# Kernel tuning notes

Hardware: AMD Instinct MI355X
Metric: run time of the kernel (lower is better)

The kernel has to match this reference:

```python
import jax, jax.numpy as jnp
import numpy as np

C_PER_GROUP = 16
T_ITERS = 5
EPS = 1e-5


def setup_inputs() -> dict:
    key = jax.random.key(0)
    k1, = jax.random.split(key, 1)
    N, C, H, W = 32, 256, 64, 64
    x = jax.random.normal(k1, (N, C, H, W), dtype=jnp.float32)
    return {
        "x": x,
        "sw_mean_weight": jnp.ones((2,), jnp.float32),
        "sw_var_weight": jnp.ones((2,), jnp.float32),
        "weight": jnp.ones((C,), jnp.float32),
        "bias": jnp.zeros((C,), jnp.float32),
    }


def reference(x, sw_mean_weight, sw_var_weight, weight, bias):
    N, C, H, W = x.shape
    c = C_PER_GROUP
    g = C // c
    HW = H * W
    NHW = N * HW

    # --- BW (batch whitening) stats over all N,H,W per group (world_size=1) ---
    # torch: x.transpose(0,1).view(g, c, N*H*W)
    xt = jnp.transpose(x, (1, 0, 2, 3)).reshape(g, c, NHW)
    mean_bn = jnp.mean(xt, axis=-1, keepdims=True)              # (g, c, 1)
    xc = xt - mean_bn
    cov_bn = jnp.einsum('gci,gdi->gcd', xc, xc) / NHW           # (g, c, c)

    # broadcast BN stats to (N*g, ...)
    mean_bn_b = jnp.broadcast_to(mean_bn[None], (N, g, c, 1)).reshape(N * g, c, 1)
    cov_bn_b = jnp.broadcast_to(cov_bn[None], (N, g, c, c)).reshape(N * g, c, c)

    # --- IW (instance whitening) stats per (sample, group) ---
    in_data = x.reshape(N * g, c, HW)
    mean_in = jnp.mean(in_data, axis=-1, keepdims=True)         # (N*g, c, 1)
    x_in = in_data - mean_in
    cov_in = jnp.einsum('bci,bdi->bcd', x_in, x_in) / HW        # (N*g, c, c)

    eye = jnp.eye(c, dtype=x.dtype)

    # --- switchable mixing (sw_type = 2: BW + IW) ---
    mw = jax.nn.softmax(sw_mean_weight)
    vw = jax.nn.softmax(sw_var_weight)
    mean = mw[0] * mean_bn_b + mw[1] * mean_in                  # (N*g, c, 1)
    cov = vw[0] * cov_bn_b + vw[1] * cov_in + EPS * eye         # (N*g, c, c)

    # --- Newton-Schulz iterative whitening ---
    trace = jnp.trace(cov, axis1=-2, axis2=-1)[:, None, None]   # (N*g, 1, 1)
    rTr = 1.0 / trace
    cov_N = cov * rTr
    P = jnp.broadcast_to(eye, cov.shape)
    for _ in range(T_ITERS):
        P3 = jnp.matmul(jnp.matmul(P, P), P)
        P = 1.5 * P - 0.5 * jnp.matmul(P3, cov_N)
    wm = P * jnp.sqrt(rTr)                                      # (N*g, c, c)

    x_hat = jnp.matmul(wm, in_data - mean).reshape(N, C, H, W)
    x_hat = x_hat * weight[None, :, None, None] + bias[None, :, None, None]
    return x_hat
```

## Files before the change

kernel.cpp:

```cpp
#include <hip/hip_runtime.h>
#include <stdint.h>

#define HWSZ 4096
#define NTRI 136
#define NSTAT 152
#define NINST 512
#define GCNT 16
#define EPSW 1e-5f
#define CHUNK 512
#define NCHUNK 8

typedef float v2f __attribute__((ext_vector_type(2)));
typedef float v4f __attribute__((ext_vector_type(4)));

typedef __attribute__((address_space(3))) float lds_f;
typedef const __attribute__((address_space(1))) float glb_f;

__device__ __forceinline__ void stage_chunk(const float* __restrict__ xb,
                                            float* bufp, int wv, int lane, int ck) {
#pragma unroll
  for (int ii = 0; ii < 8; ++ii) {
    const int d = wv * 4 + (ii >> 1);
    const int q = ii & 1;
    __builtin_amdgcn_global_load_lds(
        (glb_f*)(xb + (size_t)d * HWSZ + (size_t)ck * CHUNK + q * 256 + lane * 4),
        (lds_f*)(bufp + d * CHUNK + q * 256), 16, 0, 0);
  }
}

__global__ __launch_bounds__(256, 2) void k_inst_stats(const float* __restrict__ x,
                                                       float* __restrict__ inst_stats) {
  const int b = blockIdx.x;
  const int t = threadIdx.x;
  const int lane = t & 63;
  const int wv = t >> 6;

  __shared__ float buf[2][16 * CHUNK];
  __shared__ float red[4 * NSTAT];

  const float* xb = x + (size_t)b * 16 * HWSZ;

  float s1[16];
  float s2[NTRI];
#pragma unroll
  for (int i = 0; i < 16; ++i) s1[i] = 0.f;
#pragma unroll
  for (int i = 0; i < NTRI; ++i) s2[i] = 0.f;

  stage_chunk(xb, &buf[0][0], wv, lane, 0);
  __syncthreads();

#pragma unroll 1
  for (int ck = 0; ck < NCHUNK; ++ck) {
    if (ck + 1 < NCHUNK) stage_chunk(xb, &buf[(ck + 1) & 1][0], wv, lane, ck + 1);
    const float* bc = &buf[ck & 1][0];
    v2f v[16];
#pragma unroll
    for (int d = 0; d < 16; ++d) v[d] = *(const v2f*)&bc[d * CHUNK + 2 * t];
#pragma unroll
    for (int c = 0; c < 16; ++c) s1[c] += v[c].x + v[c].y;
    int tri = 0;
#pragma unroll
    for (int c = 0; c < 16; ++c) {
#pragma unroll
      for (int d = c; d < 16; ++d) {
        s2[tri] += v[c].x * v[d].x + v[c].y * v[d].y;
        ++tri;
      }
    }
    __syncthreads();
  }

#pragma unroll
  for (int q = 0; q < 16; ++q) {
    float v = s1[q];
#pragma unroll
    for (int off = 32; off > 0; off >>= 1) v += __shfl_down(v, off);
    if (lane == 0) red[wv * NSTAT + q] = v;
  }
#pragma unroll
  for (int q = 0; q < NTRI; ++q) {
    float v = s2[q];
#pragma unroll
    for (int off = 32; off > 0; off >>= 1) v += __shfl_down(v, off);
    if (lane == 0) red[wv * NSTAT + 16 + q] = v;
  }
  __syncthreads();
  if (t < NSTAT) {
    inst_stats[(size_t)b * NSTAT + t] =
        red[t] + red[NSTAT + t] + red[2 * NSTAT + t] + red[3 * NSTAT + t];
  }
}

__global__ __launch_bounds__(256) void k_newton(const float* __restrict__ inst_stats,
                                                const float* __restrict__ swm,
                                                const float* __restrict__ swv,
                                                const float* __restrict__ weight,
                                                const float* __restrict__ bias,
                                                float* __restrict__ apply_wm,
                                                float* __restrict__ apply_ofs) {
  const int b = blockIdx.x;
  const int g = b & 15;
  const int t = threadIdx.x;
  const int r = t >> 4;
  const int c = t & 15;

  __shared__ float P[256], Qm[256], Rm[256], CN[256], Wl[256];
  __shared__ float Mm[16], Mi[16], Mb[16];
  __shared__ float Gs[NSTAT];

  if (t < NSTAT) {
    float s = 0.f;
#pragma unroll 8
    for (int n = 0; n < 32; ++n) s += inst_stats[(size_t)(n * GCNT + g) * NSTAT + t];
    Gs[t] = s;
  }

  float a0 = swm[0], a1 = swm[1];
  float mx = fmaxf(a0, a1);
  float e0 = expf(a0 - mx), e1 = expf(a1 - mx);
  const float mw0 = e0 / (e0 + e1), mw1 = e1 / (e0 + e1);
  a0 = swv[0]; a1 = swv[1];
  mx = fmaxf(a0, a1);
  e0 = expf(a0 - mx); e1 = expf(a1 - mx);
  const float vw0 = e0 / (e0 + e1), vw1 = e1 / (e0 + e1);

  const float inv_hw = 1.0f / (float)HWSZ;
  const float inv_nhw = 1.0f / (32.0f * (float)HWSZ);

  __syncthreads();

  if (t < 16) {
    const float mi = inst_stats[(size_t)b * NSTAT + t] * inv_hw;
    const float mb = Gs[t] * inv_nhw;
    Mi[t] = mi;
    Mb[t] = mb;
    Mm[t] = mw0 * mb + mw1 * mi;
  }
  __syncthreads();

  const int cmin = (r < c) ? r : c;
  const int cmax = (r < c) ? c : r;
  const int tri = 15 * cmin - (cmin * (cmin - 1)) / 2 + cmax + 16;
  const float cin = inst_stats[(size_t)b * NSTAT + tri] * inv_hw - Mi[r] * Mi[c];
  const float cbn = Gs[tri] * inv_nhw - Mb[r] * Mb[c];
  float cov = vw0 * cbn + vw1 * cin + ((r == c) ? EPSW : 0.0f);

  Qm[t] = cov;
  __syncthreads();
  float trace = 0.f;
#pragma unroll
  for (int i = 0; i < 16; ++i) trace += Qm[i * 16 + i];
  const float rTr = 1.0f / trace;

  CN[t] = cov * rTr;
  P[t] = (r == c) ? 1.0f : 0.0f;
  __syncthreads();

  for (int it = 0; it < 5; ++it) {
    float q = 0.f;
#pragma unroll
    for (int k = 0; k < 16; ++k) q += P[r * 16 + k] * P[k * 16 + c];
    Qm[t] = q;
    __syncthreads();
    float rr = 0.f;
#pragma unroll
    for (int k = 0; k < 16; ++k) rr += Qm[r * 16 + k] * P[k * 16 + c];
    Rm[t] = rr;
    __syncthreads();
    float tt = 0.f;
#pragma unroll
    for (int k = 0; k < 16; ++k) tt += Rm[r * 16 + k] * CN[k * 16 + c];
    const float np = 1.5f * P[t] - 0.5f * tt;
    __syncthreads();
    P[t] = np;
    __syncthreads();
  }

  const float sr = sqrtf(rTr);
  const float wel = P[t] * sr * weight[g * 16 + r];
  Wl[t] = wel;
  apply_wm[(size_t)b * 256 + t] = wel;
  __syncthreads();
  if (t < 16) {
    float acc = 0.f;
#pragma unroll
    for (int d = 0; d < 16; ++d) acc += Wl[t * 16 + d] * Mm[d];
    apply_ofs[(size_t)b * 16 + t] = bias[g * 16 + t] - acc;
  }
}

__global__ __launch_bounds__(256, 4) void k_apply(const float* __restrict__ x,
                                                  const float* __restrict__ apply_wm,
                                                  const float* __restrict__ apply_ofs,
                                                  float* __restrict__ y) {
  const int bb = blockIdx.x;
  const int b = bb >> 2;
  const int chunk = bb & 3;
  const int t = threadIdx.x;

  __shared__ float Wl[256];
  __shared__ float Ol[16];
  Wl[t] = apply_wm[(size_t)b * 256 + t];
  if (t < 16) Ol[t] = apply_ofs[(size_t)b * 16 + t];
  __syncthreads();

  const v4f* xb = (const v4f*)x + (size_t)b * 16 * 1024;
  v4f* yb = (v4f*)y + (size_t)b * 16 * 1024;
  const int f = chunk * 256 + t;

  v4f v[16];
#pragma unroll
  for (int d = 0; d < 16; ++d) v[d] = xb[d * 1024 + f];

#pragma unroll
  for (int cch = 0; cch < 16; ++cch) {
    v4f acc = Ol[cch];
#pragma unroll
    for (int d = 0; d < 16; ++d) acc += Wl[cch * 16 + d] * v[d];
    yb[cch * 1024 + f] = acc;
  }
}

extern "C" void kernel_launch(void* const* d_in, const int* in_sizes, int n_in,
                              void* d_out, int out_size, void* d_ws, size_t ws_size,
                              hipStream_t stream) {
  const float* x = (const float*)d_in[0];
  const float* swm = (const float*)d_in[1];
  const float* swv = (const float*)d_in[2];
  const float* weight = (const float*)d_in[3];
  const float* bias = (const float*)d_in[4];
  float* out = (float*)d_out;

  float* ws = (float*)d_ws;
  float* inst = ws;
  float* awm = inst + (size_t)NINST * NSTAT;
  float* aofs = awm + (size_t)NINST * 256;

  k_inst_stats<<<NINST, 256, 0, stream>>>(x, inst);
  k_newton<<<NINST, 256, 0, stream>>>(inst, swm, swv, weight, bias, awm, aofs);
  k_apply<<<NINST * 4, 256, 0, stream>>>(x, awm, aofs, out);
}
```

Before: 297.5 us.

## Split covariance triangle across eight waves to cut per-thread register accumulators

The instance-stats kernel now runs 512 threads and gives each wave a balanced pair of triangle rows (row w and row 15-w). Each wave then keeps 19 accumulators per thread instead of 152, and the spatial chunk is scanned with float4 LDS reads. This removes heavy register pressure and the large shuffle reduction, which should allow higher occupancy. The cost is that every wave re-reads most channels from LDS, and a wave-indexed switch adds code size.

After: 276.0 us. 7.2% less time.

```diff
diff --git a/kernel.cpp b/kernel.cpp
--- a/kernel.cpp
+++ b/kernel.cpp
@@ -19,33 +19,52 @@
 __device__ __forceinline__ void stage_chunk(const float* __restrict__ xb,
                                             float* bufp, int wv, int lane, int ck) {
 #pragma unroll
-  for (int ii = 0; ii < 8; ++ii) {
-    const int d = wv * 4 + (ii >> 1);
+  for (int ii = 0; ii < 4; ++ii) {
+    const int ch = wv * 2 + (ii >> 1);
     const int q = ii & 1;
     __builtin_amdgcn_global_load_lds(
-        (glb_f*)(xb + (size_t)d * HWSZ + (size_t)ck * CHUNK + q * 256 + lane * 4),
-        (lds_f*)(bufp + d * CHUNK + q * 256), 16, 0, 0);
-  }
-}
-
-__global__ __launch_bounds__(256, 2) void k_inst_stats(const float* __restrict__ x,
+        (glb_f*)(xb + (size_t)ch * HWSZ + ck * CHUNK + q * 256 + lane * 4),
+        (lds_f*)(bufp + ch * CHUNK + q * 256), 16, 0, 0);
+  }
+}
+
+template <int W>
+__device__ __forceinline__ void accum_chunk(const float* bc, int lane, float acc[19]) {
+  constexpr int NCH = 16 - W;
+  constexpr int J2 = 15 - 2 * W;
+#pragma unroll
+  for (int pg = 0; pg < 2; ++pg) {
+    v4f v[NCH];
+#pragma unroll
+    for (int j = 0; j < NCH; ++j)
+      v[j] = *(const v4f*)&bc[(W + j) * CHUNK + pg * 256 + lane * 4];
+    acc[0] += (v[0].x + v[0].y) + (v[0].z + v[0].w);
+    acc[1] += (v[J2].x + v[J2].y) + (v[J2].z + v[J2].w);
+#pragma unroll
+    for (int s = 2; s <= 17 - W; ++s)
+      acc[s] += v[0].x * v[s - 2].x + v[0].y * v[s - 2].y +
+                v[0].z * v[s - 2].z + v[0].w * v[s - 2].w;
+#pragma unroll
+    for (int s = 18 - W; s <= 18; ++s)
+      acc[s] += v[J2].x * v[s - 3 - W].x + v[J2].y * v[s - 3 - W].y +
+                v[J2].z * v[s - 3 - W].z + v[J2].w * v[s - 3 - W].w;
+  }
+}
+
+__global__ __launch_bounds__(512, 4) void k_inst_stats(const float* __restrict__ x,
                                                        float* __restrict__ inst_stats) {
   const int b = blockIdx.x;
   const int t = threadIdx.x;
   const int lane = t & 63;
   const int wv = t >> 6;
-
-  __shared__ float buf[2][16 * CHUNK];
-  __shared__ float red[4 * NSTAT];
-
   const float* xb = x + (size_t)b * 16 * HWSZ;
 
-  float s1[16];
-  float s2[NTRI];
-#pragma unroll
-  for (int i = 0; i < 16; ++i) s1[i] = 0.f;
-#pragma unroll
-  for (int i = 0; i < NTRI; ++i) s2[i] = 0.f;
+  __shared__ __align__(16) float buf[2][16 * CHUNK];
+  __shared__ float red[8 * 19];
+
+  float acc[19];
+#pragma unroll
+  for (int i = 0; i < 19; ++i) acc[i] = 0.f;
 
   stage_chunk(xb, &buf[0][0], wv, lane, 0);
   __syncthreads();
@@ -54,41 +73,43 @@
   for (int ck = 0; ck < NCHUNK; ++ck) {
     if (ck + 1 < NCHUNK) stage_chunk(xb, &buf[(ck + 1) & 1][0], wv, lane, ck + 1);
     const float* bc = &buf[ck & 1][0];
-    v2f v[16];
-#pragma unroll
-    for (int d = 0; d < 16; ++d) v[d] = *(const v2f*)&bc[d * CHUNK + 2 * t];
-#pragma unroll
-    for (int c = 0; c < 16; ++c) s1[c] += v[c].x + v[c].y;
-    int tri = 0;
-#pragma unroll
-    for (int c = 0; c < 16; ++c) {
-#pragma unroll
-      for (int d = c; d < 16; ++d) {
-        s2[tri] += v[c].x * v[d].x + v[c].y * v[d].y;
-        ++tri;
-      }
+    switch (wv) {
+      case 0: accum_chunk<0>(bc, lane, acc); break;
+      case 1: accum_chunk<1>(bc, lane, acc); break;
+      case 2: accum_chunk<2>(bc, lane, acc); break;
+      case 3: accum_chunk<3>(bc, lane, acc); break;
+      case 4: accum_chunk<4>(bc, lane, acc); break;
+      case 5: accum_chunk<5>(bc, lane, acc); break;
+      case 6: accum_chunk<6>(bc, lane, acc); break;
+      default: accum_chunk<7>(bc, lane, acc); break;
     }
     __syncthreads();
   }
 
 #pragma unroll
-  for (int q = 0; q < 16; ++q) {
-    float v = s1[q];
+  for (int q = 0; q < 19; ++q) {
+    float v = acc[q];
 #pragma unroll
     for (int off = 32; off > 0; off >>= 1) v += __shfl_down(v, off);
-    if (lane == 0) red[wv * NSTAT + q] = v;
-  }
-#pragma unroll
-  for (int q = 0; q < NTRI; ++q) {
-    float v = s2[q];
-#pragma unroll
-    for (int off = 32; off > 0; off >>= 1) v += __shfl_down(v, off);
-    if (lane == 0) red[wv * NSTAT + 16 + q] = v;
-  }
-  __syncthreads();
-  if (t < NSTAT) {
-    inst_stats[(size_t)b * NSTAT + t] =
-        red[t] + red[NSTAT + t] + red[2 * NSTAT + t] + red[3 * NSTAT + t];
+    if (lane == 0) red[wv * 19 + q] = v;
+  }
+  __syncthreads();
+  if (t < 8 * 19) {
+    const int w = t / 19;
+    const int s = t - w * 19;
+    int gidx;
+    if (s == 0) {
+      gidx = w;
+    } else if (s == 1) {
+      gidx = 15 - w;
+    } else if (s <= 17 - w) {
+      const int a = w, d = w + s - 2;
+      gidx = 16 + 15 * a - (a * (a - 1)) / 2 + d;
+    } else {
+      const int a = 15 - w, d = s - 3;
+      gidx = 16 + 15 * a - (a * (a - 1)) / 2 + d;
+    }
+    inst_stats[(size_t)b * NSTAT + gidx] = red[t];
   }
 }
 
@@ -237,7 +258,7 @@
   float* awm = inst + (size_t)NINST * NSTAT;
   float* aofs = awm + (size_t)NINST * 256;
 
-  k_inst_stats<<<NINST, 256, 0, stream>>>(x, inst);
+  k_inst_stats<<<NINST, 512, 0, stream>>>(x, inst);
   k_newton<<<NINST, 256, 0, stream>>>(inst, swm, swv, weight, bias, awm, aofs);
   k_apply<<<NINST * 4, 256, 0, stream>>>(x, awm, aofs, out);
 }
```
